# Kernel optimization log

Measured on AMD Instinct MI355X. Metric: run time of the kernel, lower is better.

The kernel has to match this reference:

```python
import jax, jax.numpy as jnp
import numpy as np

K = 32          # k_value
NUM_CLASSES = 10


def setup_inputs() -> dict:
    key = jax.random.key(0)
    k1, k2, k3 = jax.random.split(key, 3)
    queries = jax.random.normal(k1, (1024, 64), dtype=jnp.float32)
    train_data = jax.random.normal(k2, (200000, 64), dtype=jnp.float32)
    train_labels = jax.random.randint(k3, (200000,), 0, NUM_CLASSES, dtype=jnp.int32)
    return {"queries": queries, "train_data": train_data, "train_labels": train_labels}


def _votes(queries, train_data, train_labels):
    # Squared Euclidean distance [Q, N] via the ||q||^2 + ||x||^2 - 2 q.x expansion
    # (same math as sum of squared differences, O(Q*N*d) without a Q*N*d temp).
    q2 = jnp.sum(queries * queries, axis=1, keepdims=True)        # [Q, 1]
    x2 = jnp.sum(train_data * train_data, axis=1)                  # [N]
    sim = q2 + x2[None, :] - 2.0 * (queries @ train_data.T)        # [Q, N]
    sim = jnp.maximum(sim, 0.0)  # exact squared distances are >= 0
    # Inversion kernel: replace exact zeros with 0.1, then weights = 1/sim.
    sim = jnp.where(sim == 0.0, jnp.float32(0.1), sim)
    weights = 1.0 / sim                                            # [Q, N]
    # Top-K weights (largest weight == nearest neighbor).
    top_w, top_i = jax.lax.top_k(weights, K)                       # [Q, K]
    top_lab = train_labels[top_i]                                  # [Q, K] int
    # segment_sum over labels == scatter-add weights per class.
    Q = queries.shape[0]
    rows = jnp.arange(Q)[:, None]                                  # [Q, 1]
    votes = jnp.zeros((Q, NUM_CLASSES), dtype=top_w.dtype).at[rows, top_lab].add(top_w)
    return votes


def reference(queries, train_data, train_labels):
    votes = _votes(queries, train_data, train_labels)
    # argmax over class weight sums == tf.argmax(segment_sum) per query
    return jnp.argmax(votes, axis=1)
```

## Files before the change

kernel.cpp:

```cpp
#include <hip/hip_runtime.h>
#include <hip/hip_bf16.h>
#include <hip/hip_fp16.h>

#define N_TRAIN 200000
#define DIMS    64
#define NQ      1024
#define KSEL    32
#define NCLS    10

#define CHROWS2 391
#define NCHUNK  512
#define NBLK0   1024
#define LCAP    8
#define OVFCAP  256
#define TOTC    4096
#define MAXS    1536
#define SAMPLES 8192
#define SROWS   64
#define NPB     3125

typedef float f32x4 __attribute__((ext_vector_type(4)));
typedef short f16x8 __attribute__((ext_vector_type(8)));

__device__ __forceinline__ unsigned fmap(float f) {
    unsigned u = __float_as_uint(f);
    return u ^ ((u >> 31) ? 0xFFFFFFFFu : 0x80000000u);
}
__device__ __forceinline__ float funmap(unsigned m) {
    unsigned u = m ^ ((m >> 31) ? 0x80000000u : 0xFFFFFFFFu);
    return __uint_as_float(u);
}
__device__ __forceinline__ unsigned short f2h(float f) {
    union { __half h; unsigned short u; } c;
    c.h = __float2half_rn(f);
    return c.u;
}
__device__ __forceinline__ f16x8 pack8h(float4 a, float4 b) {
    f16x8 r;
    r[0] = (short)f2h(a.x); r[1] = (short)f2h(a.y);
    r[2] = (short)f2h(a.z); r[3] = (short)f2h(a.w);
    r[4] = (short)f2h(b.x); r[5] = (short)f2h(b.y);
    r[6] = (short)f2h(b.z); r[7] = (short)f2h(b.w);
    return r;
}

__global__ __launch_bounds__(512) void k_prep(const float* __restrict__ X,
                                              float* __restrict__ x2,
                                              float* __restrict__ bmax,
                                              short* __restrict__ Xh) {
    int T = blockIdx.x * 512 + threadIdx.x;
    int row = T >> 3;
    int l8 = T & 7;
    const float4* xp = (const float4*)(X + (long)row * 64 + l8 * 8);
    float4 a = xp[0], b = xp[1];
    *(f16x8*)(Xh + (long)row * 64 + l8 * 8) = pack8h(a, b);
    float p = a.x * a.x + a.y * a.y + a.z * a.z + a.w * a.w +
              b.x * b.x + b.y * b.y + b.z * b.z + b.w * b.w;
    p += __shfl_xor(p, 1);
    p += __shfl_xor(p, 2);
    p += __shfl_xor(p, 4);
    if (l8 == 0) x2[row] = p;
    float m = p;
    m = fmaxf(m, __shfl_xor(m, 8));
    m = fmaxf(m, __shfl_xor(m, 16));
    m = fmaxf(m, __shfl_xor(m, 32));
    __shared__ float wm[8];
    if ((threadIdx.x & 63) == 0) wm[threadIdx.x >> 6] = m;
    __syncthreads();
    if (threadIdx.x == 0) {
        float r = wm[0];
#pragma unroll
        for (int i = 1; i < 8; i++) r = fmaxf(r, wm[i]);
        bmax[blockIdx.x] = r;
    }
}

__global__ __launch_bounds__(256) void k_max(const float* __restrict__ bmax,
                                             float* __restrict__ x2maxf) {
    float m = -1e30f;
    for (int i = threadIdx.x; i < NPB; i += 256) m = fmaxf(m, bmax[i]);
#pragma unroll
    for (int d = 1; d < 64; d <<= 1) m = fmaxf(m, __shfl_xor(m, d));
    __shared__ float wm[4];
    if ((threadIdx.x & 63) == 0) wm[threadIdx.x >> 6] = m;
    __syncthreads();
    if (threadIdx.x == 0)
        *x2maxf = fmaxf(fmaxf(wm[0], wm[1]), fmaxf(wm[2], wm[3]));
}

__global__ __launch_bounds__(256) void k_cvt(const float* __restrict__ src,
                                             short* __restrict__ dst) {
    long c = (long)blockIdx.x * 256 + threadIdx.x;
    const float4* xp = (const float4*)(src + c * 8);
    float4 a = xp[0], b = xp[1];
    *(f16x8*)(dst + c * 8) = pack8h(a, b);
}

template<int MODE>
__global__ __launch_bounds__(256) void k_dist(
    const short* __restrict__ Xh, const short* __restrict__ Qh,
    const float* __restrict__ x2, const float* __restrict__ tqw,
    unsigned* __restrict__ pcnt, unsigned* __restrict__ pool,
    unsigned* __restrict__ ovfcnt, uint2* __restrict__ ovf,
    unsigned short* __restrict__ keys) {
    int bid = blockIdx.x;
    int tid = threadIdx.x;
    int qh = bid & 1;
    int cb = bid >> 1;
    int w = tid >> 6;
    int lane = tid & 63;
    int lr = lane & 15;
    int lk = lane >> 4;

    __shared__ unsigned lcnt[MODE == 0 ? 512 : 1];
    __shared__ unsigned lbuf[MODE == 0 ? 512 * LCAP : 1];

    int r0 = MODE ? cb * SROWS : cb * CHROWS2;
    int rowEnd = MODE ? (r0 + SROWS) : min(r0 + CHROWS2, N_TRAIN);

    if (MODE == 0) {
        lcnt[tid] = 0u;
        lcnt[tid + 256] = 0u;
        __syncthreads();
    }

    int qbase = (qh << 9) + (w << 7);

    f16x8 afr[8][2];
#pragma unroll
    for (int qi = 0; qi < 8; qi++) {
        const short* qp = Qh + (long)(qbase + (qi << 4) + lr) * 64 + (lk << 3);
        afr[qi][0] = *(const f16x8*)qp;
        afr[qi][1] = *(const f16x8*)(qp + 32);
    }
    float htq[8];
    if (MODE == 0) {
#pragma unroll
        for (int qi = 0; qi < 8; qi++) {
            float4 t4 = *(const float4*)(tqw + qbase + (qi << 4) + (lk << 2));
            htq[qi] = 0.5f * fmaxf(fmaxf(t4.x, t4.y), fmaxf(t4.z, t4.w));
        }
    }

    f16x8 cb0, cb1;
    float cx2;
    {
        int rowc = min(r0 + lr, rowEnd - 1);
        const short* xp = Xh + (long)rowc * 64 + (lk << 3);
        cb0 = *(const f16x8*)xp;
        cb1 = *(const f16x8*)(xp + 32);
        cx2 = (r0 + lr < rowEnd) ? x2[rowc] : 1e30f;
    }

    for (int base = r0; base < rowEnd; base += 16) {
        f16x8 b0 = cb0, b1 = cb1;
        float x2c = cx2;
        int nb = base + 16;
        if (nb < rowEnd) {
            int rowc = min(nb + lr, rowEnd - 1);
            const short* xp = Xh + (long)rowc * 64 + (lk << 3);
            cb0 = *(const f16x8*)xp;
            cb1 = *(const f16x8*)(xp + 32);
            cx2 = (nb + lr < rowEnd) ? x2[rowc] : 1e30f;
        }
        int row = base + lr;
        bool valid = row < rowEnd;
        float hx = 0.5f * x2c;

#pragma unroll
        for (int qi = 0; qi < 8; qi++) {
            f32x4 acc = {0.f, 0.f, 0.f, 0.f};
            acc = __builtin_amdgcn_mfma_f32_16x16x32_f16(afr[qi][0], b0, acc, 0, 0, 0);
            acc = __builtin_amdgcn_mfma_f32_16x16x32_f16(afr[qi][1], b1, acc, 0, 0, 0);
            if (MODE == 1) {
#pragma unroll
                for (int r4 = 0; r4 < 4; r4++) {
                    unsigned k16 = fmap(x2c - 2.f * acc[r4]) >> 16;
                    unsigned o = (unsigned)__shfl_xor((int)k16, 1);
                    unsigned v2 = k16 | (o << 16);
                    unsigned p2 = (unsigned)__shfl_xor((int)v2, 2);
                    if ((lr & 3) == 0) {
                        int qg = qbase + (qi << 4) + (lk << 2) + r4;
                        *(uint2*)(&keys[(long)qg * SAMPLES + row]) = make_uint2(v2, p2);
                    }
                }
            } else {
                float mx = fmaxf(fmaxf(acc[0], acc[1]), fmaxf(acc[2], acc[3]));
                if (valid && mx + htq[qi] >= hx) {
                    float4 t4 = *(const float4*)(tqw + qbase + (qi << 4) + (lk << 2));
                    float tq4[4] = {t4.x, t4.y, t4.z, t4.w};
#pragma unroll
                    for (int r4 = 0; r4 < 4; r4++) {
                        if (acc[r4] + 0.5f * tq4[r4] >= hx) {
                            int qg = qbase + (qi << 4) + (lk << 2) + r4;
                            int ql = qg & 511;
                            unsigned entry = (fmap(x2c - 2.f * acc[r4]) & 0xFFFFFE00u) |
                                             (unsigned)(row - r0);
                            unsigned slot = atomicAdd(&lcnt[ql], 1u);
                            if (slot < LCAP) {
                                lbuf[ql * LCAP + slot] = entry;
                            } else {
                                unsigned o = atomicAdd(&ovfcnt[qg], 1u);
                                if (o < OVFCAP)
                                    ovf[qg * OVFCAP + o] =
                                        make_uint2(entry >> 9, (unsigned)row);
                            }
                        }
                    }
                }
            }
        }
    }

    if (MODE == 0) {
        __syncthreads();
        for (int ql = tid; ql < 512; ql += 256) {
            unsigned lc = min(lcnt[ql], (unsigned)LCAP);
            pcnt[((long)bid << 9) + ql] = lc;
            uint4 a = *(uint4*)&lbuf[ql * LCAP];
            uint4 b = *(uint4*)&lbuf[ql * LCAP + 4];
            long base = (((long)bid << 9) + ql) * LCAP;
            *(uint4*)&pool[base] = a;
            *(uint4*)&pool[base + 4] = b;
        }
    }
}

__global__ __launch_bounds__(256) void k_sel(const unsigned short* __restrict__ keys,
                                             const float* __restrict__ Qm,
                                             const float* __restrict__ x2maxf,
                                             float* __restrict__ tqw,
                                             float* __restrict__ q2g) {
    int q = blockIdx.x, tid = threadIdx.x;
    unsigned short mk[32];
#pragma unroll
    for (int m = 0; m < 32; m++) mk[m] = keys[(long)q * SAMPLES + tid + 256 * m];
    __shared__ float q2s_;
    __shared__ int cnt;
    if (tid < 64) {
        float v = Qm[(long)q * 64 + tid];
        float p = v * v;
#pragma unroll
        for (int d = 1; d < 64; d <<= 1) p += __shfl_xor(p, d);
        if (tid == 0) q2s_ = p;
    }
    unsigned lo = 0, hi = 65535;
    for (int it = 0; it < 16; ++it) {
        __syncthreads();
        if (tid == 0) cnt = 0;
        __syncthreads();
        unsigned mid = (lo + hi) >> 1;
        int c = 0;
#pragma unroll
        for (int m = 0; m < 32; m++) c += (mk[m] <= mid) ? 1 : 0;
#pragma unroll
        for (int d = 1; d < 64; d <<= 1) c += __shfl_xor(c, d);
        if ((tid & 63) == 0) atomicAdd(&cnt, c);
        __syncthreads();
        if (cnt >= KSEL) hi = mid; else lo = mid + 1;
    }
    if (tid == 0) {
        unsigned vv = hi + 2u; if (vv > 65535u) vv = 65535u;
        float t = funmap(vv << 16);
        float q2 = q2s_;
        tqw[q] = t + 0.004f * sqrtf(q2 * (*x2maxf)) + 0.1f;
        q2g[q] = q2;
    }
}

__global__ __launch_bounds__(256) void k_merge(const float* __restrict__ Qm,
                                               const float* __restrict__ X,
                                               const float* __restrict__ x2,
                                               const int* __restrict__ labels,
                                               const unsigned* __restrict__ pcnt,
                                               const unsigned* __restrict__ pool,
                                               const unsigned* __restrict__ ovfcnt,
                                               const uint2* __restrict__ ovf,
                                               const float* __restrict__ q2g,
                                               const float* __restrict__ x2maxf,
                                               int* __restrict__ out) {
    int q = blockIdx.x, tid = threadIdx.x;
    __shared__ unsigned eK[TOTC];
    __shared__ int eR[TOTC];
    __shared__ int sR[MAXS];
    __shared__ float sKey[MAXS];
    __shared__ int sLab[MAXS];
    __shared__ float qs[64];
    __shared__ int tot, cnt, ns, nw, nt;
    __shared__ unsigned cutS;
    __shared__ float wKey[34];
    __shared__ int wLab[34];
    __shared__ int tIdx[64];
    __shared__ int tLab[64];

    if (tid == 0) { tot = 0; ns = 0; nw = 0; nt = 0; }
    if (tid < 64) qs[tid] = Qm[(long)q * 64 + tid];
    __syncthreads();

    int qh = q >> 9, ql = q & 511;
    for (int c2 = tid; c2 < NCHUNK; c2 += 256) {
        int b = (c2 << 1) | qh;
        unsigned lc = pcnt[((long)b << 9) + ql];
        if (lc) {
            long base = (((long)b << 9) + ql) * LCAP;
            uint4 a = *(const uint4*)&pool[base];
            uint4 bb = *(const uint4*)&pool[base + 4];
            int p = atomicAdd(&tot, (int)lc);
            int rbase = c2 * CHROWS2;
#pragma unroll
            for (int i = 0; i < LCAP; i++) {
                unsigned e = (i == 0) ? a.x : (i == 1) ? a.y : (i == 2) ? a.z :
                             (i == 3) ? a.w : (i == 4) ? bb.x : (i == 5) ? bb.y :
                             (i == 6) ? bb.z : bb.w;
                int p2 = p + i;
                if ((unsigned)i < lc && p2 < TOTC) {
                    eK[p2] = e >> 9;
                    eR[p2] = rbase + (int)(e & 511u);
                }
            }
        }
    }
    int ov = min((int)ovfcnt[q], OVFCAP);
    for (int i = tid; i < ov; i += 256) {
        uint2 e = ovf[q * OVFCAP + i];
        int p = atomicAdd(&tot, 1);
        if (p < TOTC) { eK[p] = e.x; eR[p] = (int)e.y; }
    }
    __syncthreads();
    int T = min(tot, TOTC);

    unsigned mk[16];
#pragma unroll
    for (int m = 0; m < 16; m++) { int i = tid + (m << 8); mk[m] = (i < T) ? eK[i] : 0xFFFFFFFFu; }
    unsigned lo = 0, hi = 0x7FFFFFu;
    for (int it = 0; it < 23; ++it) {
        __syncthreads();
        if (tid == 0) cnt = 0;
        __syncthreads();
        unsigned mid = (lo + hi) >> 1;
        int c = 0;
#pragma unroll
        for (int m = 0; m < 16; m++) c += (mk[m] <= mid) ? 1 : 0;
#pragma unroll
        for (int d = 1; d < 64; d <<= 1) c += __shfl_xor(c, d);
        if ((tid & 63) == 0) atomicAdd(&cnt, c);
        __syncthreads();
        if (cnt >= KSEL) hi = mid; else lo = mid + 1;
    }
    float q2v = q2g[q];
    if (tid == 0) {
        unsigned vv = min(hi + 1u, 0x7FFFFFu);
        float tf = funmap(vv << 9);
        float err = 0.004f * sqrtf(q2v * (*x2maxf)) + 0.1f;
        cutS = min((fmap(tf + err) >> 9) + 1u, 0x7FFFFFu);
    }
    __syncthreads();
    unsigned cut = cutS;
    for (int i = tid; i < T; i += 256)
        if (eK[i] <= cut) { int p = atomicAdd(&ns, 1); if (p < MAXS) sR[p] = eR[i]; }
    __syncthreads();
    int NS = min(ns, MAXS);

    for (int i = tid; i < NS; i += 256) {
        int row = sR[i];
        const float4* xr = (const float4*)(X + (long)row * 64);
        const float4* qr = (const float4*)qs;
        float dot = 0.f;
#pragma unroll
        for (int k4 = 0; k4 < 16; k4++) {
            float4 xv = xr[k4], qv = qr[k4];
            dot += qv.x * xv.x + qv.y * xv.y + qv.z * xv.z + qv.w * xv.w;
        }
        sKey[i] = x2[row] - 2.f * dot;
        sLab[i] = labels[row];
    }
    __syncthreads();

    unsigned uk[6];
#pragma unroll
    for (int m = 0; m < 6; m++) { int i = tid + (m << 8); uk[m] = (i < NS) ? fmap(sKey[i]) : 0xFFFFFFFFu; }
    unsigned lo2 = 0u, hi2 = 0xFFFFFFFFu;
    for (int it = 0; it < 32; ++it) {
        __syncthreads();
        if (tid == 0) cnt = 0;
        __syncthreads();
        unsigned mid = lo2 + ((hi2 - lo2) >> 1);
        int c = 0;
#pragma unroll
        for (int m = 0; m < 6; m++) c += (uk[m] <= mid) ? 1 : 0;
#pragma unroll
        for (int d = 1; d < 64; d <<= 1) c += __shfl_xor(c, d);
        if ((tid & 63) == 0) atomicAdd(&cnt, c);
        __syncthreads();
        if (cnt >= KSEL) hi2 = mid; else lo2 = mid + 1;
    }
    unsigned T32 = hi2;

#pragma unroll
    for (int m = 0; m < 6; m++) {
        int i = tid + (m << 8);
        if (i < NS) {
            if (uk[m] < T32) {
                int p = atomicAdd(&nw, 1);
                if (p < 34) { wKey[p] = sKey[i]; wLab[p] = sLab[i]; }
            } else if (uk[m] == T32) {
                int p = atomicAdd(&nt, 1);
                if (p < 64) { tIdx[p] = sR[i]; tLab[p] = sLab[i]; }
            }
        }
    }
    __syncthreads();

    if (tid == 0) {
        float votes[NCLS] = {0.f, 0.f, 0.f, 0.f, 0.f, 0.f, 0.f, 0.f, 0.f, 0.f};
        int NW = min(nw, 32);
        for (int i = 0; i < NW; i++) {
            float dist = q2v + wKey[i];
            if (dist < 0.f) dist = 0.f;
            if (dist == 0.f) dist = 0.1f;
            votes[wLab[i]] += 1.f / dist;
        }
        int need = KSEL - NW;
        int NT = min(nt, 64);
        float tkey = funmap(T32);
        float dist = q2v + tkey;
        if (dist < 0.f) dist = 0.f;
        if (dist == 0.f) dist = 0.1f;
        float twgt = 1.f / dist;
        for (int t = 0; t < need && t < NT; t++) {
            int best = -1, bi = 0x7FFFFFFF;
            for (int u = 0; u < NT; u++)
                if (tIdx[u] < bi) { bi = tIdx[u]; best = u; }
            if (best < 0) break;
            votes[tLab[best]] += twgt;
            tIdx[best] = 0x7FFFFFFF;
        }
        float bv = votes[0];
        int bc = 0;
#pragma unroll
        for (int c = 1; c < NCLS; c++)
            if (votes[c] > bv) { bv = votes[c]; bc = c; }
        out[q] = bc;
    }
}

extern "C" void kernel_launch(void* const* d_in, const int* in_sizes, int n_in,
                              void* d_out, int out_size, void* d_ws, size_t ws_size,
                              hipStream_t stream) {
    const float* Qm = (const float*)d_in[0];
    const float* X = (const float*)d_in[1];
    const int* labels = (const int*)d_in[2];
    char* ws = (char*)d_ws;
    float* x2 = (float*)(ws + 0);
    float* tqw = (float*)(ws + 800000);
    float* q2g = (float*)(ws + 804096);
    float* x2maxf = (float*)(ws + 808192);
    float* bmax = (float*)(ws + 808256);
    unsigned* pcnt = (unsigned*)(ws + 820800);
    unsigned* ovfcnt = (unsigned*)(ws + 2917952);
    uint2* ovf = (uint2*)(ws + 2922048);
    unsigned short* keys = (unsigned short*)(ws + 5019200);
    unsigned* pool = (unsigned*)(ws + 5019200);
    short* Xh = (short*)(ws + 21796416);
    short* Qh = (short*)(ws + 47396416);
    int* out = (int*)d_out;

    hipMemsetAsync(ovfcnt, 0, 4096, stream);
    k_prep<<<NPB, 512, 0, stream>>>(X, x2, bmax, Xh);
    k_max<<<1, 256, 0, stream>>>(bmax, x2maxf);
    k_cvt<<<32, 256, 0, stream>>>(Qm, Qh);
    k_dist<1><<<2 * (SAMPLES / SROWS), 256, 0, stream>>>(Xh, Qh, x2, tqw, pcnt, pool, ovfcnt, ovf, keys);
    k_sel<<<NQ, 256, 0, stream>>>(keys, Qm, x2maxf, tqw, q2g);
    k_dist<0><<<NBLK0, 256, 0, stream>>>(Xh, Qh, x2, tqw, pcnt, pool, ovfcnt, ovf, keys);
    k_merge<<<NQ, 256, 0, stream>>>(Qm, X, x2, labels, pcnt, pool, ovfcnt, ovf, q2g, x2maxf, out);
}
```

Measured before the change: 252.9 us.

## Split distance kernel into single-wave blocks with smaller chunks and sentinel pool

Restructures k_dist so each block is a single 64-thread wave covering 128 queries over a 192-row chunk, giving many more, smaller blocks. The per-chunk candidate pool drops the separate count array: empty slots are filled with a sentinel and the layout becomes chunk-major per query, so merge reads one uint4 per chunk. The row offset uses 8 bits and keys 24 bits, which widens the merge bisection. The goal is better occupancy and load balance plus less pool traffic, at the cost of more blocks re-loading query fragments and a smaller local capacity (4) that may push more entries into the overflow path.

New measurement: 277.3 us. +9.7%, slower.

```diff
diff --git a/kernel.cpp b/kernel.cpp
--- a/kernel.cpp
+++ b/kernel.cpp
@@ -8,15 +8,15 @@
 #define KSEL    32
 #define NCLS    10
 
-#define CHROWS2 391
-#define NCHUNK  512
-#define NBLK0   1024
-#define LCAP    8
+#define CHR     192
+#define NCH     1042
+#define LCAP    4
+#define SENT    0xFFFFFFFFu
 #define OVFCAP  256
 #define TOTC    4096
 #define MAXS    1536
 #define SAMPLES 8192
-#define SROWS   64
+#define SROWS   32
 #define NPB     3125
 
 typedef float f32x4 __attribute__((ext_vector_type(4)));
@@ -97,34 +97,32 @@
 }
 
 template<int MODE>
-__global__ __launch_bounds__(256) void k_dist(
+__global__ __launch_bounds__(64) void k_dist(
     const short* __restrict__ Xh, const short* __restrict__ Qh,
     const float* __restrict__ x2, const float* __restrict__ tqw,
-    unsigned* __restrict__ pcnt, unsigned* __restrict__ pool,
+    unsigned* __restrict__ pool,
     unsigned* __restrict__ ovfcnt, uint2* __restrict__ ovf,
     unsigned short* __restrict__ keys) {
     int bid = blockIdx.x;
-    int tid = threadIdx.x;
-    int qh = bid & 1;
-    int cb = bid >> 1;
-    int w = tid >> 6;
-    int lane = tid & 63;
+    int qt = bid & 7;
+    int cb = bid >> 3;
+    int lane = threadIdx.x;
     int lr = lane & 15;
     int lk = lane >> 4;
 
-    __shared__ unsigned lcnt[MODE == 0 ? 512 : 1];
-    __shared__ unsigned lbuf[MODE == 0 ? 512 * LCAP : 1];
-
-    int r0 = MODE ? cb * SROWS : cb * CHROWS2;
-    int rowEnd = MODE ? (r0 + SROWS) : min(r0 + CHROWS2, N_TRAIN);
+    __shared__ unsigned lcnt[MODE == 0 ? 128 : 1];
+    __shared__ unsigned lbuf[MODE == 0 ? 128 * LCAP : 1];
+
+    int r0 = MODE ? cb * SROWS : cb * CHR;
+    int rowEnd = MODE ? (r0 + SROWS) : min(r0 + CHR, N_TRAIN);
 
     if (MODE == 0) {
-        lcnt[tid] = 0u;
-        lcnt[tid + 256] = 0u;
-        __syncthreads();
-    }
-
-    int qbase = (qh << 9) + (w << 7);
+        lcnt[lane] = 0u;
+        lcnt[lane + 64] = 0u;
+        __syncthreads();
+    }
+
+    int qbase = qt << 7;
 
     f16x8 afr[8][2];
 #pragma unroll
@@ -186,15 +184,15 @@
                 }
             } else {
                 float mx = fmaxf(fmaxf(acc[0], acc[1]), fmaxf(acc[2], acc[3]));
-                if (valid && mx + htq[qi] >= hx) {
+                if (valid && mx >= hx - htq[qi]) {
                     float4 t4 = *(const float4*)(tqw + qbase + (qi << 4) + (lk << 2));
                     float tq4[4] = {t4.x, t4.y, t4.z, t4.w};
 #pragma unroll
                     for (int r4 = 0; r4 < 4; r4++) {
-                        if (acc[r4] + 0.5f * tq4[r4] >= hx) {
-                            int qg = qbase + (qi << 4) + (lk << 2) + r4;
-                            int ql = qg & 511;
-                            unsigned entry = (fmap(x2c - 2.f * acc[r4]) & 0xFFFFFE00u) |
+                        if (acc[r4] >= hx - 0.5f * tq4[r4]) {
+                            int ql = (qi << 4) + (lk << 2) + r4;
+                            int qg = qbase + ql;
+                            unsigned entry = (fmap(x2c - 2.f * acc[r4]) & 0xFFFFFF00u) |
                                              (unsigned)(row - r0);
                             unsigned slot = atomicAdd(&lcnt[ql], 1u);
                             if (slot < LCAP) {
@@ -203,7 +201,7 @@
                                 unsigned o = atomicAdd(&ovfcnt[qg], 1u);
                                 if (o < OVFCAP)
                                     ovf[qg * OVFCAP + o] =
-                                        make_uint2(entry >> 9, (unsigned)row);
+                                        make_uint2(entry >> 8, (unsigned)row);
                             }
                         }
                     }
@@ -214,14 +212,16 @@
 
     if (MODE == 0) {
         __syncthreads();
-        for (int ql = tid; ql < 512; ql += 256) {
+#pragma unroll
+        for (int j = 0; j < 2; j++) {
+            int ql = (j << 6) + lane;
             unsigned lc = min(lcnt[ql], (unsigned)LCAP);
-            pcnt[((long)bid << 9) + ql] = lc;
-            uint4 a = *(uint4*)&lbuf[ql * LCAP];
-            uint4 b = *(uint4*)&lbuf[ql * LCAP + 4];
-            long base = (((long)bid << 9) + ql) * LCAP;
-            *(uint4*)&pool[base] = a;
-            *(uint4*)&pool[base + 4] = b;
+            uint4 v;
+            v.x = (lc > 0) ? lbuf[ql * LCAP + 0] : SENT;
+            v.y = (lc > 1) ? lbuf[ql * LCAP + 1] : SENT;
+            v.z = (lc > 2) ? lbuf[ql * LCAP + 2] : SENT;
+            v.w = (lc > 3) ? lbuf[ql * LCAP + 3] : SENT;
+            *(uint4*)&pool[((long)cb * NQ + qbase + ql) * LCAP] = v;
         }
     }
 }
@@ -272,7 +272,6 @@
                                                const float* __restrict__ X,
                                                const float* __restrict__ x2,
                                                const int* __restrict__ labels,
-                                               const unsigned* __restrict__ pcnt,
                                                const unsigned* __restrict__ pool,
                                                const unsigned* __restrict__ ovfcnt,
                                                const uint2* __restrict__ ovf,
@@ -297,28 +296,13 @@
     if (tid < 64) qs[tid] = Qm[(long)q * 64 + tid];
     __syncthreads();
 
-    int qh = q >> 9, ql = q & 511;
-    for (int c2 = tid; c2 < NCHUNK; c2 += 256) {
-        int b = (c2 << 1) | qh;
-        unsigned lc = pcnt[((long)b << 9) + ql];
-        if (lc) {
-            long base = (((long)b << 9) + ql) * LCAP;
-            uint4 a = *(const uint4*)&pool[base];
-            uint4 bb = *(const uint4*)&pool[base + 4];
-            int p = atomicAdd(&tot, (int)lc);
-            int rbase = c2 * CHROWS2;
-#pragma unroll
-            for (int i = 0; i < LCAP; i++) {
-                unsigned e = (i == 0) ? a.x : (i == 1) ? a.y : (i == 2) ? a.z :
-                             (i == 3) ? a.w : (i == 4) ? bb.x : (i == 5) ? bb.y :
-                             (i == 6) ? bb.z : bb.w;
-                int p2 = p + i;
-                if ((unsigned)i < lc && p2 < TOTC) {
-                    eK[p2] = e >> 9;
-                    eR[p2] = rbase + (int)(e & 511u);
-                }
-            }
-        }
+    for (int c2 = tid; c2 < NCH; c2 += 256) {
+        uint4 v = *(const uint4*)&pool[((long)c2 * NQ + q) * LCAP];
+        int rbase = c2 * CHR;
+        if (v.x != SENT) { int p = atomicAdd(&tot, 1); if (p < TOTC) { eK[p] = v.x >> 8; eR[p] = rbase + (int)(v.x & 255u); } }
+        if (v.y != SENT) { int p = atomicAdd(&tot, 1); if (p < TOTC) { eK[p] = v.y >> 8; eR[p] = rbase + (int)(v.y & 255u); } }
+        if (v.z != SENT) { int p = atomicAdd(&tot, 1); if (p < TOTC) { eK[p] = v.z >> 8; eR[p] = rbase + (int)(v.z & 255u); } }
+        if (v.w != SENT) { int p = atomicAdd(&tot, 1); if (p < TOTC) { eK[p] = v.w >> 8; eR[p] = rbase + (int)(v.w & 255u); } }
     }
     int ov = min((int)ovfcnt[q], OVFCAP);
     for (int i = tid; i < ov; i += 256) {
@@ -332,8 +316,8 @@
     unsigned mk[16];
 #pragma unroll
     for (int m = 0; m < 16; m++) { int i = tid + (m << 8); mk[m] = (i < T) ? eK[i] : 0xFFFFFFFFu; }
-    unsigned lo = 0, hi = 0x7FFFFFu;
-    for (int it = 0; it < 23; ++it) {
+    unsigned lo = 0, hi = 0xFFFFFFu;
+    for (int it = 0; it < 24; ++it) {
         __syncthreads();
         if (tid == 0) cnt = 0;
         __syncthreads();
@@ -349,10 +333,10 @@
     }
     float q2v = q2g[q];
     if (tid == 0) {
-        unsigned vv = min(hi + 1u, 0x7FFFFFu);
-        float tf = funmap(vv << 9);
+        unsigned vv = min(hi + 1u, 0xFFFFFFu);
+        float tf = funmap(vv << 8);
         float err = 0.004f * sqrtf(q2v * (*x2maxf)) + 0.1f;
-        cutS = min((fmap(tf + err) >> 9) + 1u, 0x7FFFFFu);
+        cutS = min((fmap(tf + err) >> 8) + 1u, 0xFFFFFFu);
     }
     __syncthreads();
     unsigned cut = cutS;
@@ -456,21 +440,20 @@
     float* q2g = (float*)(ws + 804096);
     float* x2maxf = (float*)(ws + 808192);
     float* bmax = (float*)(ws + 808256);
-    unsigned* pcnt = (unsigned*)(ws + 820800);
-    unsigned* ovfcnt = (unsigned*)(ws + 2917952);
-    uint2* ovf = (uint2*)(ws + 2922048);
-    unsigned short* keys = (unsigned short*)(ws + 5019200);
-    unsigned* pool = (unsigned*)(ws + 5019200);
-    short* Xh = (short*)(ws + 21796416);
-    short* Qh = (short*)(ws + 47396416);
+    unsigned* ovfcnt = (unsigned*)(ws + 820800);
+    uint2* ovf = (uint2*)(ws + 824896);
+    unsigned* pool = (unsigned*)(ws + 2922048);
+    unsigned short* keys = (unsigned short*)(ws + 2922048);
+    short* Xh = (short*)(ws + 19994176);
+    short* Qh = (short*)(ws + 45594176);
     int* out = (int*)d_out;
 
     hipMemsetAsync(ovfcnt, 0, 4096, stream);
     k_prep<<<NPB, 512, 0, stream>>>(X, x2, bmax, Xh);
     k_max<<<1, 256, 0, stream>>>(bmax, x2maxf);
     k_cvt<<<32, 256, 0, stream>>>(Qm, Qh);
-    k_dist<1><<<2 * (SAMPLES / SROWS), 256, 0, stream>>>(Xh, Qh, x2, tqw, pcnt, pool, ovfcnt, ovf, keys);
+    k_dist<1><<<8 * (SAMPLES / SROWS), 64, 0, stream>>>(Xh, Qh, x2, tqw, pool, ovfcnt, ovf, keys);
     k_sel<<<NQ, 256, 0, stream>>>(keys, Qm, x2maxf, tqw, q2g);
-    k_dist<0><<<NBLK0, 256, 0, stream>>>(Xh, Qh, x2, tqw, pcnt, pool, ovfcnt, ovf, keys);
-    k_merge<<<NQ, 256, 0, stream>>>(Qm, X, x2, labels, pcnt, pool, ovfcnt, ovf, q2g, x2maxf, out);
-}
+    k_dist<0><<<8 * NCH, 64, 0, stream>>>(Xh, Qh, x2, tqw, pool, ovfcnt, ovf, keys);
+    k_merge<<<NQ, 256, 0, stream>>>(Qm, X, x2, labels, pool, ovfcnt, ovf, q2g, x2maxf, out);
+}
```
